# Performance work log

Measured on AMD Instinct MI355X. Metric: run time of the kernel, lower is better.

## Reference

```python
import jax, jax.numpy as jnp
import numpy as np

N_CHEM = 200000
N_DIS = 200000
D = 256
L = 2  # num_layers
R = 4  # relations: 0=cause(chem->dis),1=relate(chem->dis),2=rev_relate(dis->chem),3=child(dis->dis)
E = 500000


def setup_inputs() -> dict:
    key = jax.random.key(0)
    ks = jax.random.split(key, 12)
    x_chem = jax.random.normal(ks[0], (N_CHEM, D), dtype=jnp.float32)
    x_dis = jax.random.normal(ks[1], (N_DIS, D), dtype=jnp.float32)
    ei_cause = jax.random.randint(ks[2], (2, E), 0, N_CHEM, dtype=jnp.int32)
    ei_relate = jax.random.randint(ks[3], (2, E), 0, N_CHEM, dtype=jnp.int32)
    ei_rev = jax.random.randint(ks[4], (2, E), 0, N_DIS, dtype=jnp.int32)
    ei_child = jax.random.randint(ks[5], (2, E), 0, N_DIS, dtype=jnp.int32)
    scale = 1.0 / np.sqrt(D)
    # PyG SAGEConv params per (layer, relation): lin_l (W+b, applied to mean-aggregated
    # neighbors) and lin_r (W only, applied to destination/root features).
    Wl = jax.random.normal(ks[6], (L, R, D, D), dtype=jnp.float32) * scale
    bl = jnp.zeros((L, R, D), dtype=jnp.float32)
    Wr = jax.random.normal(ks[7], (L, R, D, D), dtype=jnp.float32) * scale
    return {"x_chem": x_chem, "x_dis": x_dis, "Wl": Wl, "bl": bl, "Wr": Wr,
            "ei_cause": ei_cause, "ei_relate": ei_relate, "ei_rev": ei_rev,
            "ei_child": ei_child}


def _sage(x_src, x_dst, ei, Wl, bl, Wr, n_dst):
    # SAGEConv: lin_l(mean_{j in N(i)} x_j) + lin_r(x_i)
    src, dst = ei[0], ei[1]
    msg = jnp.take(x_src, src, axis=0)                      # [E, D] gather
    s = jax.ops.segment_sum(msg, dst, num_segments=n_dst)   # [n_dst, D]
    cnt = jax.ops.segment_sum(jnp.ones((ei.shape[1],), x_src.dtype), dst,
                              num_segments=n_dst)
    mean = s / jnp.maximum(cnt, 1.0)[:, None]               # zero-degree -> 0
    return mean @ Wl + bl + x_dst @ Wr


def _hetero_layer(x_chem, x_dis, Wl, bl, Wr, ei_cause, ei_relate, ei_rev, ei_child):
    # HeteroConv(aggr='sum'): sum conv outputs per destination node type.
    out_dis = (_sage(x_chem, x_dis, ei_cause, Wl[0], bl[0], Wr[0], N_DIS)
               + _sage(x_chem, x_dis, ei_relate, Wl[1], bl[1], Wr[1], N_DIS)
               + _sage(x_dis, x_dis, ei_child, Wl[3], bl[3], Wr[3], N_DIS))
    out_chem = _sage(x_dis, x_chem, ei_rev, Wl[2], bl[2], Wr[2], N_CHEM)
    return out_chem, out_dis


def reference(x_chem, x_dis, Wl, bl, Wr, ei_cause, ei_relate, ei_rev, ei_child):
    # layers[:-1]: conv -> relu -> dropout(p=0, identity)
    for l in range(L - 1):
        x_chem, x_dis = _hetero_layer(x_chem, x_dis, Wl[l], bl[l], Wr[l],
                                      ei_cause, ei_relate, ei_rev, ei_child)
        x_chem = jax.nn.relu(x_chem)
        x_dis = jax.nn.relu(x_dis)
    # last layer: conv only
    x_chem, x_dis = _hetero_layer(x_chem, x_dis, Wl[L - 1], bl[L - 1], Wr[L - 1],
                                  ei_cause, ei_relate, ei_rev, ei_child)
    return x_chem, x_dis
```

## Files before the change

kernel.cpp:

```cpp
#include <hip/hip_runtime.h>

#define D_FEAT 256
constexpr int N_CHEM = 200000;
constexpr int N_DIS  = 200000;
constexpr int N_EDGE = 500000;
constexpr int NROWS  = 200000;
constexpr int NPAD   = 200064;
constexpr int NCNT   = 4 * NROWS;
constexpr int NEALL  = 4 * N_EDGE;

typedef _Float16 f16x8 __attribute__((ext_vector_type(8)));
typedef _Float16 f16x4 __attribute__((ext_vector_type(4)));
typedef float    f32x4 __attribute__((ext_vector_type(4)));

__device__ __forceinline__ void gload_lds16(const void* g, void* l) {
    __builtin_amdgcn_global_load_lds(
        (const __attribute__((address_space(1))) void*)g,
        (__attribute__((address_space(3))) void*)l, 16, 0, 0);
}

__global__ __launch_bounds__(256) void counti_all_k(
    const int* __restrict__ e0, const int* __restrict__ e1,
    const int* __restrict__ e2, const int* __restrict__ e3,
    int* __restrict__ cnt) {
    const int g = blockIdx.x * 256 + threadIdx.x;
    if (g >= NEALL) return;
    const int r = g / N_EDGE;
    const int le = g - r * N_EDGE;
    const int* e = (r == 0) ? e0 : (r == 1) ? e1 : (r == 2) ? e2 : e3;
    atomicAdd(&cnt[r * NROWS + e[N_EDGE + le]], 1);
}

__global__ __launch_bounds__(256) void scan1_k(const int* __restrict__ cnt,
                                               int* __restrict__ offs,
                                               int* __restrict__ bsums, int n) {
    __shared__ int s[256];
    const int t = threadIdx.x;
    const int i = blockIdx.x * 256 + t;
    const int v = (i < n) ? cnt[i] : 0;
    s[t] = v;
    __syncthreads();
#pragma unroll
    for (int d = 1; d < 256; d <<= 1) {
        const int x = (t >= d) ? s[t - d] : 0;
        __syncthreads();
        s[t] += x;
        __syncthreads();
    }
    if (i < n) offs[i] = s[t] - v;
    if (t == 255) bsums[blockIdx.x] = s[255];
}

__global__ __launch_bounds__(1024) void scan2_k(int* __restrict__ bsums, int nb) {
    __shared__ int s[1024];
    const int t = threadIdx.x;
    int v[4];
    int sum = 0;
#pragma unroll
    for (int q = 0; q < 4; ++q) {
        const int i = t * 4 + q;
        v[q] = (i < nb) ? bsums[i] : 0;
        sum += v[q];
    }
    s[t] = sum;
    __syncthreads();
#pragma unroll
    for (int d = 1; d < 1024; d <<= 1) {
        const int x = (t >= d) ? s[t - d] : 0;
        __syncthreads();
        s[t] += x;
        __syncthreads();
    }
    int base = s[t] - sum;
#pragma unroll
    for (int q = 0; q < 4; ++q) {
        const int i = t * 4 + q;
        if (i < nb) {
            const int tmp = v[q];
            bsums[i] = base;
            base += tmp;
        }
    }
}

__global__ __launch_bounds__(256) void scan3_k(int* __restrict__ offs,
                                               int* __restrict__ cursor,
                                               const int* __restrict__ bsums, int n) {
    const int i = blockIdx.x * 256 + threadIdx.x;
    if (i < n) {
        const int v = offs[i] + bsums[blockIdx.x];
        offs[i] = v;
        cursor[i] = v;
    }
}

__global__ __launch_bounds__(256) void fill_all_k(
    const int* __restrict__ e0, const int* __restrict__ e1,
    const int* __restrict__ e2, const int* __restrict__ e3,
    int* __restrict__ cursor, int* __restrict__ csr) {
    const int g = blockIdx.x * 256 + threadIdx.x;
    if (g >= NEALL) return;
    const int r = g / N_EDGE;
    const int le = g - r * N_EDGE;
    const int* e = (r == 0) ? e0 : (r == 1) ? e1 : (r == 2) ? e2 : e3;
    const int d = e[N_EDGE + le];
    const int p = atomicAdd(&cursor[r * NROWS + d], 1);
    csr[p] = e[le];
}

__global__ __launch_bounds__(256) void wt_k(const float* __restrict__ Wl,
                                            const float* __restrict__ Wr,
                                            const float* __restrict__ bl,
                                            _Float16* __restrict__ WT_dis,
                                            _Float16* __restrict__ WT_chem,
                                            float* __restrict__ bsum) {
    const int idx = blockIdx.x * 256 + threadIdx.x;
    const int l = blockIdx.y;
    const float* Wl_l = Wl + (size_t)l * 4 * 65536;
    const float* Wr_l = Wr + (size_t)l * 4 * 65536;
    if (idx < 262144) {
        const int n = idx >> 10, k = idx & 1023, seg = k >> 8, kk = k & 255;
        float v;
        if (seg == 0)
            v = Wr_l[kk * 256 + n] + Wr_l[65536 + kk * 256 + n] + Wr_l[3 * 65536 + kk * 256 + n];
        else if (seg == 1) v = Wl_l[kk * 256 + n];
        else if (seg == 2) v = Wl_l[65536 + kk * 256 + n];
        else               v = Wl_l[3 * 65536 + kk * 256 + n];
        WT_dis[(size_t)l * 262144 + idx] = (_Float16)v;
    } else if (idx < 393216) {
        const int li = idx - 262144;
        const int n = li >> 9, k = li & 511, seg = k >> 8, kk = k & 255;
        const float v = (seg == 0) ? Wr_l[2 * 65536 + kk * 256 + n]
                                   : Wl_l[2 * 65536 + kk * 256 + n];
        WT_chem[(size_t)l * 131072 + li] = (_Float16)v;
    } else if (idx < 393216 + 256) {
        const int n = idx - 393216;
        const float* b = bl + (size_t)l * 1024;
        bsum[l * 256 + n] = b[n] + b[256 + n] + b[3 * 256 + n];
    }
}

__global__ __launch_bounds__(256) void cvt2_k(const float* __restrict__ in0,
                                              _Float16* __restrict__ out0,
                                              const float* __restrict__ in1,
                                              _Float16* __restrict__ out1, int n4) {
    const int i = blockIdx.x * 256 + threadIdx.x;
    const float* in = blockIdx.y ? in1 : in0;
    _Float16* out = blockIdx.y ? out1 : out0;
    if (i < n4) {
        const float4 v = reinterpret_cast<const float4*>(in)[i];
        f16x4 o;
        o[0] = (_Float16)v.x; o[1] = (_Float16)v.y;
        o[2] = (_Float16)v.z; o[3] = (_Float16)v.w;
        reinterpret_cast<f16x4*>(out)[i] = o;
    }
}

__global__ __launch_bounds__(256) void gather_all_k(
    const _Float16* __restrict__ srcA, const _Float16* __restrict__ srcB,
    const int* __restrict__ csr, const int* __restrict__ offs,
    const int* __restrict__ cnt, _Float16* __restrict__ chunkbuf,
    int crp, int base, int rows) {
    const int y = blockIdx.y;
    const int rel = (y == 0) ? 0 : (y == 1) ? 1 : (y == 2) ? 3 : 2;
    const _Float16* x = (y < 2) ? srcA : srcB;
    _Float16* agg = chunkbuf + (size_t)y * crp * D_FEAT;
    const int* offs_r = offs + rel * NROWS;
    const int* cnt_r  = cnt + rel * NROWS;

    const int wid = threadIdx.x >> 6;
    const int lane = threadIdx.x & 63;
    const int grp = lane >> 4;
    const int li  = lane & 15;
    const int lrow = blockIdx.x * 16 + wid * 4 + grp;
    if (lrow >= rows) return;
    const int row = base + lrow;
    const int start = offs_r[row];
    const int n = cnt_r[row];
    float a0[8] = {0,0,0,0,0,0,0,0}, a1[8] = {0,0,0,0,0,0,0,0};
    const _Float16* xb = x + li * 16;
    int j = 0;
    for (; j + 2 <= n; j += 2) {
        const int s0 = csr[start + j];
        const int s1 = csr[start + j + 1];
        const f16x8 u0 = *reinterpret_cast<const f16x8*>(xb + (size_t)s0 * D_FEAT);
        const f16x8 u1 = *reinterpret_cast<const f16x8*>(xb + (size_t)s0 * D_FEAT + 8);
        const f16x8 w0 = *reinterpret_cast<const f16x8*>(xb + (size_t)s1 * D_FEAT);
        const f16x8 w1 = *reinterpret_cast<const f16x8*>(xb + (size_t)s1 * D_FEAT + 8);
#pragma unroll
        for (int q = 0; q < 8; ++q) {
            a0[q] += (float)u0[q]; a1[q] += (float)u1[q];
            a0[q] += (float)w0[q]; a1[q] += (float)w1[q];
        }
    }
    if (j < n) {
        const int s0 = csr[start + j];
        const f16x8 u0 = *reinterpret_cast<const f16x8*>(xb + (size_t)s0 * D_FEAT);
        const f16x8 u1 = *reinterpret_cast<const f16x8*>(xb + (size_t)s0 * D_FEAT + 8);
#pragma unroll
        for (int q = 0; q < 8; ++q) { a0[q] += (float)u0[q]; a1[q] += (float)u1[q]; }
    }
    const float inv = 1.0f / fmaxf((float)n, 1.0f);
    f16x8 o0, o1;
#pragma unroll
    for (int q = 0; q < 8; ++q) {
        o0[q] = (_Float16)(a0[q] * inv);
        o1[q] = (_Float16)(a1[q] * inv);
    }
    _Float16* ap = agg + (size_t)lrow * D_FEAT + li * 16;
    *reinterpret_cast<f16x8*>(ap) = o0;
    *reinterpret_cast<f16x8*>(ap + 8) = o1;
}

template <int NSEG, bool RELU_OUT>
__device__ __forceinline__ void gemm_body(
    _Float16* __restrict__ AslBase, _Float16* __restrict__ BslBase,
    const _Float16* __restrict__ A0, const _Float16* __restrict__ A1,
    const _Float16* __restrict__ A2, const _Float16* __restrict__ A3,
    const _Float16* __restrict__ WT, const float* __restrict__ bias,
    float* __restrict__ Cf, _Float16* __restrict__ Ch, int vrows) {
    constexpr int KT = NSEG * 256;
    constexpr int NS = KT / 64;
    const int t = threadIdx.x;
    const int w = t >> 6, l = t & 63;
    const int wm = w & 1, wn = w >> 1;
    const int fr = l & 15, ko = (l >> 4) << 3;
    const int row0 = blockIdx.x * 128;
    const int col0 = blockIdx.y * 128;

    f32x4 acc[4][4];
#pragma unroll
    for (int m = 0; m < 4; ++m)
#pragma unroll
        for (int n = 0; n < 4; ++n) acc[m][n] = f32x4{0.f, 0.f, 0.f, 0.f};

    const int srow = t >> 3;
    const int schk = t & 7;
    const int gchk = schk ^ (srow & 7);
    const int rsw  = (fr & 7) << 3;

    auto STAGE = [&](int buf, int ks) {
        const int seg = ks >> 2;
        const _Float16* Ab = (seg == 0) ? A0 : ((seg == 1) ? A1 : ((seg == 2) ? A2 : A3));
        const int kofs = ((ks & 3) << 6) + gchk * 8;
        _Float16* asl = AslBase + buf * 8192;
        _Float16* bsl = BslBase + buf * 8192;
#pragma unroll
        for (int is = 0; is < 4; ++is) {
            gload_lds16(Ab + (size_t)(row0 + is * 32 + srow) * D_FEAT + kofs,
                        asl + is * 2048 + w * 512);
            gload_lds16(WT + (size_t)(col0 + is * 32 + srow) * KT + seg * 256 + kofs,
                        bsl + is * 2048 + w * 512);
        }
    };

    auto COMPUTE = [&](int buf) {
        const _Float16* asl = AslBase + buf * 8192;
        const _Float16* bsl = BslBase + buf * 8192;
#pragma unroll
        for (int kk = 0; kk < 64; kk += 32) {
            f16x8 af[4], bf[4];
            const int ksw = (kk + ko) ^ rsw;
#pragma unroll
            for (int m = 0; m < 4; ++m)
                af[m] = *reinterpret_cast<const f16x8*>(&asl[(wm * 64 + m * 16 + fr) * 64 + ksw]);
#pragma unroll
            for (int n = 0; n < 4; ++n)
                bf[n] = *reinterpret_cast<const f16x8*>(&bsl[(wn * 64 + n * 16 + fr) * 64 + ksw]);
#pragma unroll
            for (int m = 0; m < 4; ++m)
#pragma unroll
                for (int n = 0; n < 4; ++n)
                    acc[m][n] = __builtin_amdgcn_mfma_f32_16x16x32_f16(af[m], bf[n], acc[m][n], 0, 0, 0);
        }
    };

    STAGE(0, 0);
    int cur = 0;
    for (int ks = 0; ks < NS - 1; ++ks) {
        STAGE(cur ^ 1, ks + 1);
        asm volatile("s_waitcnt vmcnt(8)" ::: "memory");
        __builtin_amdgcn_s_barrier();
        __builtin_amdgcn_sched_barrier(0);
        COMPUTE(cur);
        __builtin_amdgcn_sched_barrier(0);
        __builtin_amdgcn_s_barrier();
        __builtin_amdgcn_sched_barrier(0);
        cur ^= 1;
    }
    asm volatile("s_waitcnt vmcnt(0)" ::: "memory");
    __builtin_amdgcn_s_barrier();
    __builtin_amdgcn_sched_barrier(0);
    COMPUTE(cur);

    const int cro = (l >> 4) << 2;
#pragma unroll
    for (int n = 0; n < 4; ++n) {
        const int col = col0 + wn * 64 + n * 16 + fr;
        const float bi = bias[col];
#pragma unroll
        for (int m = 0; m < 4; ++m) {
            const int rbase = row0 + wm * 64 + m * 16 + cro;
#pragma unroll
            for (int j = 0; j < 4; ++j) {
                const int r = rbase + j;
                if (r < vrows) {
                    const float v = acc[m][n][j] + bi;
                    if constexpr (RELU_OUT)
                        Ch[(size_t)r * D_FEAT + col] = (_Float16)fmaxf(v, 0.f);
                    else
                        Cf[(size_t)r * D_FEAT + col] = v;
                }
            }
        }
    }
}

template <bool RELU_OUT>
__global__ __launch_bounds__(256) void gemm2_k(
    const _Float16* __restrict__ A0d, const _Float16* __restrict__ A1,
    const _Float16* __restrict__ A2, const _Float16* __restrict__ A3,
    const _Float16* __restrict__ WTd, const float* __restrict__ biasd,
    float* __restrict__ Cfd, _Float16* __restrict__ Chd,
    const _Float16* __restrict__ A0c, const _Float16* __restrict__ A4,
    const _Float16* __restrict__ WTc, const float* __restrict__ biasc,
    float* __restrict__ Cfc, _Float16* __restrict__ Chc, int vrows) {
    __shared__ _Float16 Asl[2 * 128 * 64];
    __shared__ _Float16 Bsl[2 * 128 * 64];
    if (blockIdx.z == 0)
        gemm_body<4, RELU_OUT>(Asl, Bsl, A0d, A1, A2, A3, WTd, biasd, Cfd, Chd, vrows);
    else
        gemm_body<2, RELU_OUT>(Asl, Bsl, A0c, A4, nullptr, nullptr, WTc, biasc, Cfc, Chc, vrows);
}

extern "C" void kernel_launch(void* const* d_in, const int* in_sizes, int n_in,
                              void* d_out, int out_size, void* d_ws, size_t ws_size,
                              hipStream_t stream) {
    const float* x_chem = (const float*)d_in[0];
    const float* x_dis  = (const float*)d_in[1];
    const float* Wl     = (const float*)d_in[2];
    const float* bl     = (const float*)d_in[3];
    const float* Wr     = (const float*)d_in[4];
    const int* ei[4] = {(const int*)d_in[5],
                        (const int*)d_in[6],
                        (const int*)d_in[7],
                        (const int*)d_in[8]};

    float* out_chem = (float*)d_out;
    float* out_dis  = out_chem + (size_t)N_CHEM * D_FEAT;

    constexpr size_t FB = (size_t)NPAD * D_FEAT * 2;
    char* w = (char*)d_ws;
    _Float16* h_chem  = (_Float16*)(w);
    _Float16* h_dis   = (_Float16*)(w + FB);
    _Float16* xb_chem = (_Float16*)(w + 2 * FB);
    _Float16* xb_dis  = (_Float16*)(w + 3 * FB);
    char* p = w + 4 * FB;
    int* csr    = (int*)(p);              p += 8000000;
    int* counts = (int*)(p);              p += 3200000;
    int* offs   = (int*)(p);              p += 3200000;
    int* cursor = (int*)(p);              p += 3200000;
    int* bsums  = (int*)(p);              p += 16384;
    _Float16* WT_dis  = (_Float16*)(p);   p += 1048576;
    _Float16* WT_chem = (_Float16*)(p);   p += 524288;
    float* bsum = (float*)(p);            p += 2048;
    _Float16* chunkbuf = (_Float16*)(p);

    const size_t FIXED = (size_t)(p - w);
    long long avail = (long long)ws_size - (long long)FIXED;
    int crp = 51200;
    if (avail < (long long)crp * 2048) {
        long long c = avail / 2048;
        if (c > NPAD) c = NPAD;
        crp = (int)(c & ~127LL);
        if (crp < 128) crp = 128;
    }

    const int eall_grid = (NEALL + 255) / 256;
    const int scan_blocks = (NCNT + 255) / 256;
    hipMemsetAsync(counts, 0, NCNT * sizeof(int), stream);
    counti_all_k<<<eall_grid, 256, 0, stream>>>(ei[0], ei[1], ei[2], ei[3], counts);
    scan1_k<<<scan_blocks, 256, 0, stream>>>(counts, offs, bsums, NCNT);
    scan2_k<<<1, 1024, 0, stream>>>(bsums, scan_blocks);
    scan3_k<<<scan_blocks, 256, 0, stream>>>(offs, cursor, bsums, NCNT);
    fill_all_k<<<eall_grid, 256, 0, stream>>>(ei[0], ei[1], ei[2], ei[3], cursor, csr);

    wt_k<<<dim3(1538, 2), 256, 0, stream>>>(Wl, Wr, bl, WT_dis, WT_chem, bsum);
    const int cvt_grid = (NROWS * (D_FEAT / 4) + 255) / 256;
    cvt2_k<<<dim3(cvt_grid, 2), 256, 0, stream>>>(x_chem, xb_chem, x_dis, xb_dis,
                                                  NROWS * (D_FEAT / 4));

    _Float16* slot0 = chunkbuf;
    _Float16* slot1 = chunkbuf + (size_t)1 * crp * D_FEAT;
    _Float16* slot2 = chunkbuf + (size_t)2 * crp * D_FEAT;
    _Float16* slot3 = chunkbuf + (size_t)3 * crp * D_FEAT;

    for (int base = 0; base < NROWS; base += crp) {
        const int rows = (NROWS - base < crp) ? (NROWS - base) : crp;
        const int rows_pad = (rows + 127) & ~127;
        const dim3 ggrid((rows + 15) / 16, 4);
        const dim3 mgrid(rows_pad / 128, 2, 2);
        gather_all_k<<<ggrid, 256, 0, stream>>>(xb_chem, xb_dis, csr, offs, counts,
                                                chunkbuf, crp, base, rows);
        gemm2_k<true><<<mgrid, 256, 0, stream>>>(
            xb_dis + (size_t)base * D_FEAT, slot0, slot1, slot2,
            WT_dis, bsum, nullptr, h_dis + (size_t)base * D_FEAT,
            xb_chem + (size_t)base * D_FEAT, slot3,
            WT_chem, bl + 2 * 256, nullptr, h_chem + (size_t)base * D_FEAT, rows);
    }

    for (int base = 0; base < NROWS; base += crp) {
        const int rows = (NROWS - base < crp) ? (NROWS - base) : crp;
        const int rows_pad = (rows + 127) & ~127;
        const dim3 ggrid((rows + 15) / 16, 4);
        const dim3 mgrid(rows_pad / 128, 2, 2);
        gather_all_k<<<ggrid, 256, 0, stream>>>(h_chem, h_dis, csr, offs, counts,
                                                chunkbuf, crp, base, rows);
        gemm2_k<false><<<mgrid, 256, 0, stream>>>(
            h_dis + (size_t)base * D_FEAT, slot0, slot1, slot2,
            WT_dis + 262144, bsum + 256, out_dis + (size_t)base * D_FEAT, nullptr,
            h_chem + (size_t)base * D_FEAT, slot3,
            WT_chem + 131072, bl + 6 * 256, out_chem + (size_t)base * D_FEAT, nullptr, rows);
    }
}
```

Measured before the change: 1.599 ms.

## Fuse prep kernels, drop scan3 pass, and unroll gather by four

Merges edge counting, fp32-to-fp16 feature conversion and weight transposition into one prep launch. Removes the scan3 pass by writing local offsets into the cursor and adding the block-prefix sums at use time in fill and gather. Unrolls the neighbor gather loop to four edges per iteration, using clamped indices and zero weights for the tail, to raise memory-level parallelism. This costs redundant loads and FMAs on the tail and an extra bsums lookup per row or edge.

```diff
diff --git a/kernel.cpp b/kernel.cpp
--- a/kernel.cpp
+++ b/kernel.cpp
@@ -9,6 +9,10 @@
 constexpr int NCNT   = 4 * NROWS;
 constexpr int NEALL  = 4 * N_EDGE;
 
+constexpr int PB_CNT = (NEALL + 255) / 256;
+constexpr int PB_CVT = NROWS * D_FEAT / 4 / 256;
+constexpr int PB_WT  = 1538;
+
 typedef _Float16 f16x8 __attribute__((ext_vector_type(8)));
 typedef _Float16 f16x4 __attribute__((ext_vector_type(4)));
 typedef float    f32x4 __attribute__((ext_vector_type(4)));
@@ -19,20 +23,66 @@
         (__attribute__((address_space(3))) void*)l, 16, 0, 0);
 }
 
-__global__ __launch_bounds__(256) void counti_all_k(
+__global__ __launch_bounds__(256) void prep_k(
     const int* __restrict__ e0, const int* __restrict__ e1,
     const int* __restrict__ e2, const int* __restrict__ e3,
-    int* __restrict__ cnt) {
-    const int g = blockIdx.x * 256 + threadIdx.x;
-    if (g >= NEALL) return;
-    const int r = g / N_EDGE;
-    const int le = g - r * N_EDGE;
-    const int* e = (r == 0) ? e0 : (r == 1) ? e1 : (r == 2) ? e2 : e3;
-    atomicAdd(&cnt[r * NROWS + e[N_EDGE + le]], 1);
+    int* __restrict__ cnt,
+    const float* __restrict__ x_chem, _Float16* __restrict__ xb_chem,
+    const float* __restrict__ x_dis,  _Float16* __restrict__ xb_dis,
+    const float* __restrict__ Wl, const float* __restrict__ Wr,
+    const float* __restrict__ bl,
+    _Float16* __restrict__ WT_dis, _Float16* __restrict__ WT_chem,
+    float* __restrict__ bsum) {
+    const int b = blockIdx.x;
+    if (b < PB_CNT) {
+        const int g = b * 256 + threadIdx.x;
+        if (g >= NEALL) return;
+        const int r = g / N_EDGE;
+        const int le = g - r * N_EDGE;
+        const int* e = (r == 0) ? e0 : (r == 1) ? e1 : (r == 2) ? e2 : e3;
+        atomicAdd(&cnt[r * NROWS + e[N_EDGE + le]], 1);
+    } else if (b < PB_CNT + 2 * PB_CVT) {
+        const int b1 = b - PB_CNT;
+        const float* in = (b1 < PB_CVT) ? x_chem : x_dis;
+        _Float16* out = (b1 < PB_CVT) ? xb_chem : xb_dis;
+        const int i = (b1 % PB_CVT) * 256 + threadIdx.x;
+        const float4 v = reinterpret_cast<const float4*>(in)[i];
+        f16x4 o;
+        o[0] = (_Float16)v.x; o[1] = (_Float16)v.y;
+        o[2] = (_Float16)v.z; o[3] = (_Float16)v.w;
+        reinterpret_cast<f16x4*>(out)[i] = o;
+    } else {
+        const int b2 = b - PB_CNT - 2 * PB_CVT;
+        const int l = b2 / PB_WT;
+        const int idx = (b2 % PB_WT) * 256 + threadIdx.x;
+        const float* Wl_l = Wl + (size_t)l * 4 * 65536;
+        const float* Wr_l = Wr + (size_t)l * 4 * 65536;
+        if (idx < 262144) {
+            const int n = idx >> 10, k = idx & 1023, seg = k >> 8, kk = k & 255;
+            float v;
+            if (seg == 0)
+                v = Wr_l[kk * 256 + n] + Wr_l[65536 + kk * 256 + n] + Wr_l[3 * 65536 + kk * 256 + n];
+            else if (seg == 1) v = Wl_l[kk * 256 + n];
+            else if (seg == 2) v = Wl_l[65536 + kk * 256 + n];
+            else               v = Wl_l[3 * 65536 + kk * 256 + n];
+            WT_dis[(size_t)l * 262144 + idx] = (_Float16)v;
+        } else if (idx < 393216) {
+            const int li = idx - 262144;
+            const int n = li >> 9, k = li & 511, seg = k >> 8, kk = k & 255;
+            const float v = (seg == 0) ? Wr_l[2 * 65536 + kk * 256 + n]
+                                       : Wl_l[2 * 65536 + kk * 256 + n];
+            WT_chem[(size_t)l * 131072 + li] = (_Float16)v;
+        } else if (idx < 393216 + 256) {
+            const int n = idx - 393216;
+            const float* bb = bl + (size_t)l * 1024;
+            bsum[l * 256 + n] = bb[n] + bb[256 + n] + bb[3 * 256 + n];
+        }
+    }
 }
 
 __global__ __launch_bounds__(256) void scan1_k(const int* __restrict__ cnt,
                                                int* __restrict__ offs,
+                                               int* __restrict__ cursor,
                                                int* __restrict__ bsums, int n) {
     __shared__ int s[256];
     const int t = threadIdx.x;
@@ -47,7 +97,11 @@
         s[t] += x;
         __syncthreads();
     }
-    if (i < n) offs[i] = s[t] - v;
+    if (i < n) {
+        const int o = s[t] - v;
+        offs[i] = o;
+        cursor[i] = o;
+    }
     if (t == 255) bsums[blockIdx.x] = s[255];
 }
 
@@ -83,90 +137,30 @@
     }
 }
 
-__global__ __launch_bounds__(256) void scan3_k(int* __restrict__ offs,
-                                               int* __restrict__ cursor,
-                                               const int* __restrict__ bsums, int n) {
-    const int i = blockIdx.x * 256 + threadIdx.x;
-    if (i < n) {
-        const int v = offs[i] + bsums[blockIdx.x];
-        offs[i] = v;
-        cursor[i] = v;
-    }
-}
-
 __global__ __launch_bounds__(256) void fill_all_k(
     const int* __restrict__ e0, const int* __restrict__ e1,
     const int* __restrict__ e2, const int* __restrict__ e3,
-    int* __restrict__ cursor, int* __restrict__ csr) {
+    int* __restrict__ cursor, const int* __restrict__ bsums,
+    int* __restrict__ csr) {
     const int g = blockIdx.x * 256 + threadIdx.x;
     if (g >= NEALL) return;
     const int r = g / N_EDGE;
     const int le = g - r * N_EDGE;
     const int* e = (r == 0) ? e0 : (r == 1) ? e1 : (r == 2) ? e2 : e3;
-    const int d = e[N_EDGE + le];
-    const int p = atomicAdd(&cursor[r * NROWS + d], 1);
+    const int d = r * NROWS + e[N_EDGE + le];
+    const int p = atomicAdd(&cursor[d], 1) + bsums[d >> 8];
     csr[p] = e[le];
-}
-
-__global__ __launch_bounds__(256) void wt_k(const float* __restrict__ Wl,
-                                            const float* __restrict__ Wr,
-                                            const float* __restrict__ bl,
-                                            _Float16* __restrict__ WT_dis,
-                                            _Float16* __restrict__ WT_chem,
-                                            float* __restrict__ bsum) {
-    const int idx = blockIdx.x * 256 + threadIdx.x;
-    const int l = blockIdx.y;
-    const float* Wl_l = Wl + (size_t)l * 4 * 65536;
-    const float* Wr_l = Wr + (size_t)l * 4 * 65536;
-    if (idx < 262144) {
-        const int n = idx >> 10, k = idx & 1023, seg = k >> 8, kk = k & 255;
-        float v;
-        if (seg == 0)
-            v = Wr_l[kk * 256 + n] + Wr_l[65536 + kk * 256 + n] + Wr_l[3 * 65536 + kk * 256 + n];
-        else if (seg == 1) v = Wl_l[kk * 256 + n];
-        else if (seg == 2) v = Wl_l[65536 + kk * 256 + n];
-        else               v = Wl_l[3 * 65536 + kk * 256 + n];
-        WT_dis[(size_t)l * 262144 + idx] = (_Float16)v;
-    } else if (idx < 393216) {
-        const int li = idx - 262144;
-        const int n = li >> 9, k = li & 511, seg = k >> 8, kk = k & 255;
-        const float v = (seg == 0) ? Wr_l[2 * 65536 + kk * 256 + n]
-                                   : Wl_l[2 * 65536 + kk * 256 + n];
-        WT_chem[(size_t)l * 131072 + li] = (_Float16)v;
-    } else if (idx < 393216 + 256) {
-        const int n = idx - 393216;
-        const float* b = bl + (size_t)l * 1024;
-        bsum[l * 256 + n] = b[n] + b[256 + n] + b[3 * 256 + n];
-    }
-}
-
-__global__ __launch_bounds__(256) void cvt2_k(const float* __restrict__ in0,
-                                              _Float16* __restrict__ out0,
-                                              const float* __restrict__ in1,
-                                              _Float16* __restrict__ out1, int n4) {
-    const int i = blockIdx.x * 256 + threadIdx.x;
-    const float* in = blockIdx.y ? in1 : in0;
-    _Float16* out = blockIdx.y ? out1 : out0;
-    if (i < n4) {
-        const float4 v = reinterpret_cast<const float4*>(in)[i];
-        f16x4 o;
-        o[0] = (_Float16)v.x; o[1] = (_Float16)v.y;
-        o[2] = (_Float16)v.z; o[3] = (_Float16)v.w;
-        reinterpret_cast<f16x4*>(out)[i] = o;
-    }
 }
 
 __global__ __launch_bounds__(256) void gather_all_k(
     const _Float16* __restrict__ srcA, const _Float16* __restrict__ srcB,
     const int* __restrict__ csr, const int* __restrict__ offs,
-    const int* __restrict__ cnt, _Float16* __restrict__ chunkbuf,
-    int crp, int base, int rows) {
+    const int* __restrict__ bsums, const int* __restrict__ cnt,
+    _Float16* __restrict__ chunkbuf, int crp, int base, int rows) {
     const int y = blockIdx.y;
     const int rel = (y == 0) ? 0 : (y == 1) ? 1 : (y == 2) ? 3 : 2;
     const _Float16* x = (y < 2) ? srcA : srcB;
     _Float16* agg = chunkbuf + (size_t)y * crp * D_FEAT;
-    const int* offs_r = offs + rel * NROWS;
-    const int* cnt_r  = cnt + rel * NROWS;
 
     const int wid = threadIdx.x >> 6;
     const int lane = threadIdx.x & 63;
@@ -174,31 +168,43 @@
     const int li  = lane & 15;
     const int lrow = blockIdx.x * 16 + wid * 4 + grp;
     if (lrow >= rows) return;
-    const int row = base + lrow;
-    const int start = offs_r[row];
-    const int n = cnt_r[row];
+    const int g = rel * NROWS + base + lrow;
+    const int start = offs[g] + bsums[g >> 8];
+    const int n = cnt[g];
     float a0[8] = {0,0,0,0,0,0,0,0}, a1[8] = {0,0,0,0,0,0,0,0};
     const _Float16* xb = x + li * 16;
-    int j = 0;
-    for (; j + 2 <= n; j += 2) {
-        const int s0 = csr[start + j];
-        const int s1 = csr[start + j + 1];
-        const f16x8 u0 = *reinterpret_cast<const f16x8*>(xb + (size_t)s0 * D_FEAT);
-        const f16x8 u1 = *reinterpret_cast<const f16x8*>(xb + (size_t)s0 * D_FEAT + 8);
-        const f16x8 w0 = *reinterpret_cast<const f16x8*>(xb + (size_t)s1 * D_FEAT);
-        const f16x8 w1 = *reinterpret_cast<const f16x8*>(xb + (size_t)s1 * D_FEAT + 8);
+    for (int j = 0; j < n; j += 4) {
+        const int rem = n - j;
+        const int i0 = start + j;
+        const int c1 = (rem > 1) ? 1 : 0;
+        const int c2 = (rem > 2) ? 2 : 0;
+        const int c3 = (rem > 3) ? 3 : 0;
+        const int s0 = csr[i0];
+        const int s1 = csr[i0 + c1];
+        const int s2 = csr[i0 + c2];
+        const int s3 = csr[i0 + c3];
+        const float w1 = c1 ? 1.f : 0.f;
+        const float w2 = c2 ? 1.f : 0.f;
+        const float w3 = c3 ? 1.f : 0.f;
+        const f16x8 u0a = *reinterpret_cast<const f16x8*>(xb + (size_t)s0 * D_FEAT);
+        const f16x8 u0b = *reinterpret_cast<const f16x8*>(xb + (size_t)s0 * D_FEAT + 8);
+        const f16x8 u1a = *reinterpret_cast<const f16x8*>(xb + (size_t)s1 * D_FEAT);
+        const f16x8 u1b = *reinterpret_cast<const f16x8*>(xb + (size_t)s1 * D_FEAT + 8);
+        const f16x8 u2a = *reinterpret_cast<const f16x8*>(xb + (size_t)s2 * D_FEAT);
+        const f16x8 u2b = *reinterpret_cast<const f16x8*>(xb + (size_t)s2 * D_FEAT + 8);
+        const f16x8 u3a = *reinterpret_cast<const f16x8*>(xb + (size_t)s3 * D_FEAT);
+        const f16x8 u3b = *reinterpret_cast<const f16x8*>(xb + (size_t)s3 * D_FEAT + 8);
 #pragma unroll
         for (int q = 0; q < 8; ++q) {
-            a0[q] += (float)u0[q]; a1[q] += (float)u1[q];
-            a0[q] += (float)w0[q]; a1[q] += (float)w1[q];
-        }
-    }
-    if (j < n) {
-        const int s0 = csr[start + j];
-        const f16x8 u0 = *reinterpret_cast<const f16x8*>(xb + (size_t)s0 * D_FEAT);
-        const f16x8 u1 = *reinterpret_cast<const f16x8*>(xb + (size_t)s0 * D_FEAT + 8);
-#pragma unroll
-        for (int q = 0; q < 8; ++q) { a0[q] += (float)u0[q]; a1[q] += (float)u1[q]; }
+            a0[q] += (float)u0a[q];
+            a0[q] = fmaf(w1, (float)u1a[q], a0[q]);
+            a0[q] = fmaf(w2, (float)u2a[q], a0[q]);
+            a0[q] = fmaf(w3, (float)u3a[q], a0[q]);
+            a1[q] += (float)u0b[q];
+            a1[q] = fmaf(w1, (float)u1b[q], a1[q]);
+            a1[q] = fmaf(w2, (float)u2b[q], a1[q]);
+            a1[q] = fmaf(w3, (float)u3b[q], a1[q]);
+        }
     }
     const float inv = 1.0f / fmaxf((float)n, 1.0f);
     f16x8 o0, o1;
@@ -379,16 +385,12 @@
     const int eall_grid = (NEALL + 255) / 256;
     const int scan_blocks = (NCNT + 255) / 256;
     hipMemsetAsync(counts, 0, NCNT * sizeof(int), stream);
-    counti_all_k<<<eall_grid, 256, 0, stream>>>(ei[0], ei[1], ei[2], ei[3], counts);
-    scan1_k<<<scan_blocks, 256, 0, stream>>>(counts, offs, bsums, NCNT);
+    prep_k<<<PB_CNT + 2 * PB_CVT + 2 * PB_WT, 256, 0, stream>>>(
+        ei[0], ei[1], ei[2], ei[3], counts,
+        x_chem, xb_chem, x_dis, xb_dis, Wl, Wr, bl, WT_dis, WT_chem, bsum);
+    scan1_k<<<scan_blocks, 256, 0, stream>>>(counts, offs, cursor, bsums, NCNT);
     scan2_k<<<1, 1024, 0, stream>>>(bsums, scan_blocks);
-    scan3_k<<<scan_blocks, 256, 0, stream>>>(offs, cursor, bsums, NCNT);
-    fill_all_k<<<eall_grid, 256, 0, stream>>>(ei[0], ei[1], ei[2], ei[3], cursor, csr);
-
-    wt_k<<<dim3(1538, 2), 256, 0, stream>>>(Wl, Wr, bl, WT_dis, WT_chem, bsum);
-    const int cvt_grid = (NROWS * (D_FEAT / 4) + 255) / 256;
-    cvt2_k<<<dim3(cvt_grid, 2), 256, 0, stream>>>(x_chem, xb_chem, x_dis, xb_dis,
-                                                  NROWS * (D_FEAT / 4));
+    fill_all_k<<<eall_grid, 256, 0, stream>>>(ei[0], ei[1], ei[2], ei[3], cursor, bsums, csr);
 
     _Float16* slot0 = chunkbuf;
     _Float16* slot1 = chunkbuf + (size_t)1 * crp * D_FEAT;
@@ -400,8 +402,8 @@
         const int rows_pad = (rows + 127) & ~127;
         const dim3 ggrid((rows + 15) / 16, 4);
         const dim3 mgrid(rows_pad / 128, 2, 2);
-        gather_all_k<<<ggrid, 256, 0, stream>>>(xb_chem, xb_dis, csr, offs, counts,
-                                                chunkbuf, crp, base, rows);
+        gather_all_k<<<ggrid, 256, 0, stream>>>(xb_chem, xb_dis, csr, offs, bsums,
+                                                counts, chunkbuf, crp, base, rows);
         gemm2_k<true><<<mgrid, 256, 0, stream>>>(
             xb_dis + (size_t)base * D_FEAT, slot0, slot1, slot2,
             WT_dis, bsum, nullptr, h_dis + (size_t)base * D_FEAT,
@@ -414,8 +416,8 @@
         const int rows_pad = (rows + 127) & ~127;
         const dim3 ggrid((rows + 15) / 16, 4);
         const dim3 mgrid(rows_pad / 128, 2, 2);
-        gather_all_k<<<ggrid, 256, 0, stream>>>(h_chem, h_dis, csr, offs, counts,
-                                                chunkbuf, crp, base, rows);
+        gather_all_k<<<ggrid, 256, 0, stream>>>(h_chem, h_dis, csr, offs, bsums,
+                                                counts, chunkbuf, crp, base, rows);
         gemm2_k<false><<<mgrid, 256, 0, stream>>>(
             h_dis + (size_t)base * D_FEAT, slot0, slot1, slot2,
             WT_dis + 262144, bsum + 256, out_dis + (size_t)base * D_FEAT, nullptr,
```

After: 1.587 ms. Within noise of the previous version (-0.7%).
